# Performance work log

Hardware: AMD Instinct MI355X
Metric: run time of the kernel (lower is better)

The kernel has to match this reference:

```python
import jax, jax.numpy as jnp
import numpy as np

N, D = 16384, 512
MARGIN = 2.0
EPS = 1e-6  # torch TripletMarginLoss default eps added inside pairwise distance


def setup_inputs() -> dict:
    key = jax.random.key(0)
    k1, k2 = jax.random.split(key)
    inputs = jax.random.normal(k1, (N, D), dtype=jnp.float32)
    positive = jax.random.normal(k2, (N, D), dtype=jnp.float32)
    return {"inputs": inputs, "positive": positive}


def reference(inputs, positive):
    # pairwise squared euclidean distances: ||xi||^2 + ||xj||^2 - 2 xi.xj
    sq = jnp.sum(inputs * inputs, axis=1)                      # [n]
    dist2 = sq[:, None] + sq[None, :] - 2.0 * (inputs @ inputs.T)  # [n,n]
    dist = jnp.sqrt(jnp.clip(dist2, 1e-12))                    # [n,n]
    # original does full argsort per row but only uses index 2 (3rd smallest);
    # top_k on negated distances selects the 3 smallest efficiently.
    _, idx3 = jax.lax.top_k(-dist, 3)                          # [n,3]
    negative = inputs[idx3[:, 2]]                              # [n,d]
    # TripletMarginLoss(margin, p=2): mean(relu(||a-p+eps|| - ||a-n+eps|| + m))
    d_ap = jnp.linalg.norm(inputs - positive + EPS, axis=1)
    d_an = jnp.linalg.norm(inputs - negative + EPS, axis=1)
    loss = jnp.mean(jnp.maximum(d_ap - d_an + MARGIN, 0.0))
    return loss
```

## Files before the change

### kernel.cpp

```cpp
#include <hip/hip_runtime.h>
#include <hip/hip_bf16.h>
#include <hip/hip_fp8.h>
#include <stdint.h>

#define NN 16384
#define DD 512
#define MARGINV 2.0f
#define EPSV 1e-6f

#define BJ 32
#define JGROUPS 8
#define JRANGE (NN / JGROUPS)
#define NTILES (JRANGE / BJ)
#define ROWQ 512
#define TILEB (BJ * ROWQ)
#define SQOFF (2 * TILEB)

#define KEYMASK  0xFFFFC000
#define KEYINITF __builtin_bit_cast(float, 0x7F000000)
#define BIASV 640.0f

typedef __attribute__((ext_vector_type(4))) float f32x4;
typedef __attribute__((ext_vector_type(4))) int   i32x4;
typedef __attribute__((ext_vector_type(8))) int   i32x8;

#define UNIT_SCALE 0x7F

__device__ inline void kins3f(float u, float& m0, float& m1, float& m2) {
  m2 = __builtin_amdgcn_fmed3f(m1, m2, u);
  m1 = __builtin_amdgcn_fmed3f(m0, m1, u);
  m0 = fminf(m0, u);
}

extern "C" __global__ __launch_bounds__(256)
void prep_kernel(const float* __restrict__ x, unsigned char* __restrict__ xq,
                 float* __restrict__ sqb, float* __restrict__ out) {
  if (blockIdx.x == 0 && threadIdx.x == 0) out[0] = 0.0f;
  int row  = blockIdx.x * 4 + (threadIdx.x >> 6);
  int lane = threadIdx.x & 63;
  const float* xr = x + (size_t)row * DD + lane * 8;
  f32x4 a = *(const f32x4*)xr;
  f32x4 b = *(const f32x4*)(xr + 4);
  float s = a[0]*a[0]+a[1]*a[1]+a[2]*a[2]+a[3]*a[3]
          + b[0]*b[0]+b[1]*b[1]+b[2]*b[2]+b[3]*b[3];
  #pragma unroll
  for (int off = 1; off < 64; off <<= 1) s += __shfl_xor(s, off, 64);
  unsigned long long pk = 0;
  #pragma unroll
  for (int t = 0; t < 4; ++t) {
    __hip_fp8_e4m3 qa(a[t]), qb(b[t]);
    pk |= ((unsigned long long)qa.__x) << (8 * t);
    pk |= ((unsigned long long)qb.__x) << (8 * (t + 4));
  }
  *(unsigned long long*)(xq + (size_t)row * ROWQ + lane * 8) = pk;
  if (lane == 0) sqb[row] = s + BIASV;
}

extern "C" __global__ __launch_bounds__(256, 2)
void knn_kernel(const unsigned char* __restrict__ xq, const float* __restrict__ sqb,
                int* __restrict__ pk) {
  __shared__ __align__(16) char lds[2 * TILEB + 8192];
  const int tid  = threadIdx.x;
  const int wave = tid >> 6;
  const int lane = tid & 63;
  const int quad = lane >> 4;
  const int r16  = lane & 15;
  const int bi   = blockIdx.x >> 3;
  const int bj   = blockIdx.x & 7;
  const int ibase = bi * 256 + wave * 64;
  const int jbase = bj * JRANGE;

  #pragma unroll
  for (int p = 0; p < 2; ++p) {
    const float* gs = sqb + jbase + p * 1024 + wave * 256 + lane * 4;
    char* ld = lds + SQOFF + p * 4096 + wave * 1024;
    __builtin_amdgcn_global_load_lds((const __attribute__((address_space(1))) void*)gs,
                                     (__attribute__((address_space(3))) void*)ld,
                                     16, 0, 0);
  }

  i32x8 afr[4][4];
  #pragma unroll
  for (int s = 0; s < 4; ++s) {
    const unsigned char* ar = xq + (size_t)(ibase + s * 16 + r16) * ROWQ + quad * 32;
    #pragma unroll
    for (int c = 0; c < 4; ++c)
      afr[s][c] = *(const i32x8*)(ar + c * 128);
  }

  float m0[16], m1[16], m2[16];
  #pragma unroll
  for (int q = 0; q < 16; ++q) { m0[q] = m1[q] = m2[q] = KEYINITF; }

  auto stage = [&](int jt, int buf) {
    const int jrow0 = jbase + jt * BJ;
    #pragma unroll
    for (int p = 0; p < 4; ++p) {
      const int rr = wave * 8 + p * 2;
      const int lr = rr + (lane >> 5);
      const int u  = (lane & 31) ^ (lr & 7);
      const unsigned char* gsrc = xq + (size_t)(jrow0 + lr) * ROWQ + u * 16;
      char* ldst = lds + buf * TILEB + rr * ROWQ;
      __builtin_amdgcn_global_load_lds((const __attribute__((address_space(1))) void*)gsrc,
                                       (__attribute__((address_space(3))) void*)ldst,
                                       16, 0, 0);
    }
  };

  const int sw = r16 & 7;
  stage(0, 0);
  for (int jt = 0; jt < NTILES; ++jt) {
    __syncthreads();
    if (jt + 1 < NTILES) stage(jt + 1, (jt + 1) & 1);
    #pragma unroll
    for (int jh = 0; jh < 2; ++jh) {
      const char* brow = lds + (jt & 1) * TILEB + (jh * 16 + r16) * ROWQ;
      const float sqj = *(const float*)(lds + SQOFF + ((jt * BJ + jh * 16 + r16) << 2));
      f32x4 acc[4] = {{0.f,0.f,0.f,0.f},{0.f,0.f,0.f,0.f},
                      {0.f,0.f,0.f,0.f},{0.f,0.f,0.f,0.f}};
      #pragma unroll
      for (int c = 0; c < 4; ++c) {
        const int g0 = c * 8 + quad * 2;
        i32x4 lo = *(const i32x4*)(brow + ((g0       ^ sw) * 16));
        i32x4 hi = *(const i32x4*)(brow + (((g0 + 1) ^ sw) * 16));
        i32x8 bf = i32x8{lo[0],lo[1],lo[2],lo[3],hi[0],hi[1],hi[2],hi[3]};
        #pragma unroll
        for (int s = 0; s < 4; ++s)
          acc[s] = __builtin_amdgcn_mfma_scale_f32_16x16x128_f8f6f4(
                     afr[s][c], bf, acc[s], 0, 0, 0, UNIT_SCALE, 0, UNIT_SCALE);
      }
      const int j = jbase + jt * BJ + jh * 16 + r16;
      #pragma unroll
      for (int s = 0; s < 4; ++s) {
        #pragma unroll
        for (int r = 0; r < 4; ++r) {
          float v = fmaf(-2.0f, acc[s][r], sqj);
          int   b = (__builtin_bit_cast(int, v) & KEYMASK) | j;
          kins3f(__builtin_bit_cast(float, b), m0[s*4+r], m1[s*4+r], m2[s*4+r]);
        }
      }
    }
  }

  #pragma unroll
  for (int m = 1; m <= 8; m <<= 1) {
    #pragma unroll
    for (int q = 0; q < 16; ++q) {
      float o0 = __shfl_xor(m0[q], m, 64);
      float o1 = __shfl_xor(m1[q], m, 64);
      float o2 = __shfl_xor(m2[q], m, 64);
      kins3f(o0, m0[q], m1[q], m2[q]);
      kins3f(o1, m0[q], m1[q], m2[q]);
      kins3f(o2, m0[q], m1[q], m2[q]);
    }
  }

  #pragma unroll
  for (int q = 0; q < 16; ++q) {
    if (r16 == q) {
      int s  = q >> 2, r = q & 3;
      int gi = ibase + s * 16 + quad * 4 + r;
      int ob = (gi * JGROUPS + bj) * 3;
      pk[ob + 0] = __builtin_bit_cast(int, m0[q]);
      pk[ob + 1] = __builtin_bit_cast(int, m1[q]);
      pk[ob + 2] = __builtin_bit_cast(int, m2[q]);
    }
  }
}

extern "C" __global__ __launch_bounds__(256)
void finalize_kernel(const float* __restrict__ x, const float* __restrict__ pos,
                     const int* __restrict__ pk, float* __restrict__ out) {
  __shared__ float wsum[4];
  int wave = threadIdx.x >> 6;
  int lane = threadIdx.x & 63;
  float acc = 0.f;
  #pragma unroll
  for (int rep = 0; rep < 8; ++rep) {
    int i = rep * 2048 + blockIdx.x * 4 + wave;
    int neg = 0;
    if (lane == 0) {
      float m0 = KEYINITF, m1 = KEYINITF, m2 = KEYINITF;
      #pragma unroll
      for (int s = 0; s < JGROUPS * 3; ++s) {
        kins3f(__builtin_bit_cast(float, pk[i * (JGROUPS * 3) + s]), m0, m1, m2);
      }
      neg = __builtin_bit_cast(int, m2) & 0x3FFF;
    }
    neg = __shfl(neg, 0, 64);
    const float* xr = x   + (size_t)i * DD + lane * 8;
    const float* pr = pos + (size_t)i * DD + lane * 8;
    const float* nr = x   + (size_t)neg * DD + lane * 8;
    f32x4 xa = *(const f32x4*)xr, xb4 = *(const f32x4*)(xr + 4);
    f32x4 pa = *(const f32x4*)pr, pb  = *(const f32x4*)(pr + 4);
    f32x4 na = *(const f32x4*)nr, nb  = *(const f32x4*)(nr + 4);
    float sap = 0.f, san = 0.f;
    #pragma unroll
    for (int k = 0; k < 4; ++k) {
      float d0 = xa[k]  - pa[k] + EPSV; sap = fmaf(d0, d0, sap);
      float d1 = xa[k]  - na[k] + EPSV; san = fmaf(d1, d1, san);
      float d2 = xb4[k] - pb[k] + EPSV; sap = fmaf(d2, d2, sap);
      float d3 = xb4[k] - nb[k] + EPSV; san = fmaf(d3, d3, san);
    }
    #pragma unroll
    for (int off = 1; off < 64; off <<= 1) {
      sap += __shfl_xor(sap, off, 64);
      san += __shfl_xor(san, off, 64);
    }
    if (lane == 0) {
      float l = sqrtf(sap) - sqrtf(san) + MARGINV;
      acc += (l > 0.f ? l : 0.f);
    }
  }
  if (lane == 0) wsum[wave] = acc;
  __syncthreads();
  if (threadIdx.x == 0) {
    atomicAdd(out, (wsum[0] + wsum[1] + wsum[2] + wsum[3]) * (1.0f / NN));
  }
}

extern "C" void kernel_launch(void* const* d_in, const int* in_sizes, int n_in,
                              void* d_out, int out_size, void* d_ws, size_t ws_size,
                              hipStream_t stream) {
  const float* x   = (const float*)d_in[0];
  const float* pos = (const float*)d_in[1];
  char* ws = (char*)d_ws;
  unsigned char* xq  = (unsigned char*)ws;
  float* sqb = (float*)(ws + (size_t)NN * ROWQ);
  int*   pk  = (int*)  (ws + (size_t)NN * ROWQ + (size_t)NN * 4);

  prep_kernel<<<NN / 4, 256, 0, stream>>>(x, xq, sqb, (float*)d_out);
  knn_kernel<<<(NN / 256) * JGROUPS, 256, 0, stream>>>(xq, sqb, pk);
  finalize_kernel<<<512, 256, 0, stream>>>(x, pos, pk, (float*)d_out);
}
```

Before: 237.0 us.

## Track top-2 excluding self, use 8-wave blocks, hardware FP8 pack, deterministic reduce

The kNN kernel now runs 512-thread blocks in which each wave handles 32 rows instead of 64. It masks the diagonal so each row keeps only the two smallest non-self keys instead of three, which removes one med3 per candidate and shrinks register state. It also raises MFMA issue priority with setprio. The prep kernel uses the hardware packed FP8 conversion instead of per-element conversion. Finalize merges the 16 partial keys with a wave shuffle and writes per-block partials that a new single-block reduce kernel sums, replacing the atomic. Self-exclusion assumes the self-distance is always the minimum, which matches the reference's index-2 choice unless there are duplicates or near ties.

```diff
diff --git a/kernel.cpp b/kernel.cpp
--- a/kernel.cpp
+++ b/kernel.cpp
@@ -26,16 +26,14 @@
 
 #define UNIT_SCALE 0x7F
 
-__device__ inline void kins3f(float u, float& m0, float& m1, float& m2) {
-  m2 = __builtin_amdgcn_fmed3f(m1, m2, u);
+__device__ inline void kins2f(float u, float& m0, float& m1) {
   m1 = __builtin_amdgcn_fmed3f(m0, m1, u);
   m0 = fminf(m0, u);
 }
 
 extern "C" __global__ __launch_bounds__(256)
 void prep_kernel(const float* __restrict__ x, unsigned char* __restrict__ xq,
-                 float* __restrict__ sqb, float* __restrict__ out) {
-  if (blockIdx.x == 0 && threadIdx.x == 0) out[0] = 0.0f;
+                 float* __restrict__ sqb) {
   int row  = blockIdx.x * 4 + (threadIdx.x >> 6);
   int lane = threadIdx.x & 63;
   const float* xr = x + (size_t)row * DD + lane * 8;
@@ -45,18 +43,16 @@
           + b[0]*b[0]+b[1]*b[1]+b[2]*b[2]+b[3]*b[3];
   #pragma unroll
   for (int off = 1; off < 64; off <<= 1) s += __shfl_xor(s, off, 64);
-  unsigned long long pk = 0;
-  #pragma unroll
-  for (int t = 0; t < 4; ++t) {
-    __hip_fp8_e4m3 qa(a[t]), qb(b[t]);
-    pk |= ((unsigned long long)qa.__x) << (8 * t);
-    pk |= ((unsigned long long)qb.__x) << (8 * (t + 4));
-  }
-  *(unsigned long long*)(xq + (size_t)row * ROWQ + lane * 8) = pk;
+  unsigned int w0 = (unsigned int)__builtin_amdgcn_cvt_pk_fp8_f32(a[0], a[1], 0, false);
+  w0 = (unsigned int)__builtin_amdgcn_cvt_pk_fp8_f32(a[2], a[3], (int)w0, true);
+  unsigned int w1 = (unsigned int)__builtin_amdgcn_cvt_pk_fp8_f32(b[0], b[1], 0, false);
+  w1 = (unsigned int)__builtin_amdgcn_cvt_pk_fp8_f32(b[2], b[3], (int)w1, true);
+  unsigned long long pk8 = ((unsigned long long)w1 << 32) | (unsigned long long)w0;
+  *(unsigned long long*)(xq + (size_t)row * ROWQ + lane * 8) = pk8;
   if (lane == 0) sqb[row] = s + BIASV;
 }
 
-extern "C" __global__ __launch_bounds__(256, 2)
+extern "C" __global__ __launch_bounds__(512, 4)
 void knn_kernel(const unsigned char* __restrict__ xq, const float* __restrict__ sqb,
                 int* __restrict__ pk) {
   __shared__ __align__(16) char lds[2 * TILEB + 8192];
@@ -67,36 +63,35 @@
   const int r16  = lane & 15;
   const int bi   = blockIdx.x >> 3;
   const int bj   = blockIdx.x & 7;
-  const int ibase = bi * 256 + wave * 64;
+  const int ibase = bi * 256 + wave * 32;
   const int jbase = bj * JRANGE;
 
-  #pragma unroll
-  for (int p = 0; p < 2; ++p) {
-    const float* gs = sqb + jbase + p * 1024 + wave * 256 + lane * 4;
-    char* ld = lds + SQOFF + p * 4096 + wave * 1024;
+  {
+    const float* gs = sqb + jbase + wave * 256 + lane * 4;
+    char* ld = lds + SQOFF + wave * 1024;
     __builtin_amdgcn_global_load_lds((const __attribute__((address_space(1))) void*)gs,
                                      (__attribute__((address_space(3))) void*)ld,
                                      16, 0, 0);
   }
 
-  i32x8 afr[4][4];
-  #pragma unroll
-  for (int s = 0; s < 4; ++s) {
+  i32x8 afr[2][4];
+  #pragma unroll
+  for (int s = 0; s < 2; ++s) {
     const unsigned char* ar = xq + (size_t)(ibase + s * 16 + r16) * ROWQ + quad * 32;
     #pragma unroll
     for (int c = 0; c < 4; ++c)
       afr[s][c] = *(const i32x8*)(ar + c * 128);
   }
 
-  float m0[16], m1[16], m2[16];
-  #pragma unroll
-  for (int q = 0; q < 16; ++q) { m0[q] = m1[q] = m2[q] = KEYINITF; }
+  float m0[8], m1[8];
+  #pragma unroll
+  for (int q = 0; q < 8; ++q) { m0[q] = m1[q] = KEYINITF; }
 
   auto stage = [&](int jt, int buf) {
     const int jrow0 = jbase + jt * BJ;
     #pragma unroll
-    for (int p = 0; p < 4; ++p) {
-      const int rr = wave * 8 + p * 2;
+    for (int p = 0; p < 2; ++p) {
+      const int rr = wave * 4 + p * 2;
       const int lr = rr + (lane >> 5);
       const int u  = (lane & 31) ^ (lr & 7);
       const unsigned char* gsrc = xq + (size_t)(jrow0 + lr) * ROWQ + u * 16;
@@ -112,31 +107,45 @@
   for (int jt = 0; jt < NTILES; ++jt) {
     __syncthreads();
     if (jt + 1 < NTILES) stage(jt + 1, (jt + 1) & 1);
+    const bool diagt = ((bi >> 3) == bj) && ((jt >> 3) == (bi & 7));
     #pragma unroll
     for (int jh = 0; jh < 2; ++jh) {
       const char* brow = lds + (jt & 1) * TILEB + (jh * 16 + r16) * ROWQ;
       const float sqj = *(const float*)(lds + SQOFF + ((jt * BJ + jh * 16 + r16) << 2));
-      f32x4 acc[4] = {{0.f,0.f,0.f,0.f},{0.f,0.f,0.f,0.f},
-                      {0.f,0.f,0.f,0.f},{0.f,0.f,0.f,0.f}};
+      f32x4 acc[2] = {{0.f,0.f,0.f,0.f},{0.f,0.f,0.f,0.f}};
       #pragma unroll
       for (int c = 0; c < 4; ++c) {
         const int g0 = c * 8 + quad * 2;
         i32x4 lo = *(const i32x4*)(brow + ((g0       ^ sw) * 16));
         i32x4 hi = *(const i32x4*)(brow + (((g0 + 1) ^ sw) * 16));
         i32x8 bf = i32x8{lo[0],lo[1],lo[2],lo[3],hi[0],hi[1],hi[2],hi[3]};
-        #pragma unroll
-        for (int s = 0; s < 4; ++s)
+        __builtin_amdgcn_s_setprio(1);
+        #pragma unroll
+        for (int s = 0; s < 2; ++s)
           acc[s] = __builtin_amdgcn_mfma_scale_f32_16x16x128_f8f6f4(
                      afr[s][c], bf, acc[s], 0, 0, 0, UNIT_SCALE, 0, UNIT_SCALE);
+        __builtin_amdgcn_s_setprio(0);
       }
       const int j = jbase + jt * BJ + jh * 16 + r16;
-      #pragma unroll
-      for (int s = 0; s < 4; ++s) {
+      if (diagt) {
+        #pragma unroll
+        for (int s = 0; s < 2; ++s)
         #pragma unroll
         for (int r = 0; r < 4; ++r) {
           float v = fmaf(-2.0f, acc[s][r], sqj);
           int   b = (__builtin_bit_cast(int, v) & KEYMASK) | j;
-          kins3f(__builtin_bit_cast(float, b), m0[s*4+r], m1[s*4+r], m2[s*4+r]);
+          float u = __builtin_bit_cast(float, b);
+          u = (j == (ibase + s * 16 + quad * 4 + r)) ? KEYINITF : u;
+          kins2f(u, m0[s*4+r], m1[s*4+r]);
+        }
+      } else {
+        #pragma unroll
+        for (int s = 0; s < 2; ++s)
+        #pragma unroll
+        for (int r = 0; r < 4; ++r) {
+          float v = fmaf(-2.0f, acc[s][r], sqj);
+          int   b = (__builtin_bit_cast(int, v) & KEYMASK) | j;
+          kins2f(__builtin_bit_cast(float, b), m0[s*4+r], m1[s*4+r]);
         }
       }
     }
@@ -145,49 +154,47 @@
   #pragma unroll
   for (int m = 1; m <= 8; m <<= 1) {
     #pragma unroll
-    for (int q = 0; q < 16; ++q) {
+    for (int q = 0; q < 8; ++q) {
       float o0 = __shfl_xor(m0[q], m, 64);
       float o1 = __shfl_xor(m1[q], m, 64);
-      float o2 = __shfl_xor(m2[q], m, 64);
-      kins3f(o0, m0[q], m1[q], m2[q]);
-      kins3f(o1, m0[q], m1[q], m2[q]);
-      kins3f(o2, m0[q], m1[q], m2[q]);
-    }
-  }
-
-  #pragma unroll
-  for (int q = 0; q < 16; ++q) {
+      kins2f(o0, m0[q], m1[q]);
+      kins2f(o1, m0[q], m1[q]);
+    }
+  }
+
+  #pragma unroll
+  for (int q = 0; q < 8; ++q) {
     if (r16 == q) {
       int s  = q >> 2, r = q & 3;
       int gi = ibase + s * 16 + quad * 4 + r;
-      int ob = (gi * JGROUPS + bj) * 3;
+      int ob = (gi * JGROUPS + bj) * 2;
       pk[ob + 0] = __builtin_bit_cast(int, m0[q]);
       pk[ob + 1] = __builtin_bit_cast(int, m1[q]);
-      pk[ob + 2] = __builtin_bit_cast(int, m2[q]);
     }
   }
 }
 
 extern "C" __global__ __launch_bounds__(256)
 void finalize_kernel(const float* __restrict__ x, const float* __restrict__ pos,
-                     const int* __restrict__ pk, float* __restrict__ out) {
+                     const int* __restrict__ pk, float* __restrict__ partial) {
   __shared__ float wsum[4];
   int wave = threadIdx.x >> 6;
   int lane = threadIdx.x & 63;
   float acc = 0.f;
   #pragma unroll
-  for (int rep = 0; rep < 8; ++rep) {
-    int i = rep * 2048 + blockIdx.x * 4 + wave;
-    int neg = 0;
-    if (lane == 0) {
-      float m0 = KEYINITF, m1 = KEYINITF, m2 = KEYINITF;
-      #pragma unroll
-      for (int s = 0; s < JGROUPS * 3; ++s) {
-        kins3f(__builtin_bit_cast(float, pk[i * (JGROUPS * 3) + s]), m0, m1, m2);
-      }
-      neg = __builtin_bit_cast(int, m2) & 0x3FFF;
-    }
-    neg = __shfl(neg, 0, 64);
+  for (int rep = 0; rep < 2; ++rep) {
+    int i = rep * 8192 + blockIdx.x * 4 + wave;
+    float m0 = (lane < 16) ? __builtin_bit_cast(float, pk[i * 16 + lane]) : KEYINITF;
+    float m1 = KEYINITF;
+    #pragma unroll
+    for (int m = 1; m <= 8; m <<= 1) {
+      float o0 = __shfl_xor(m0, m, 64);
+      float o1 = __shfl_xor(m1, m, 64);
+      float t0 = fminf(m0, o0);
+      m1 = fminf(fmaxf(m0, o0), fminf(m1, o1));
+      m0 = t0;
+    }
+    int neg = __shfl(__builtin_bit_cast(int, m1), 0, 64) & 0x3FFF;
     const float* xr = x   + (size_t)i * DD + lane * 8;
     const float* pr = pos + (size_t)i * DD + lane * 8;
     const float* nr = x   + (size_t)neg * DD + lane * 8;
@@ -214,9 +221,21 @@
   }
   if (lane == 0) wsum[wave] = acc;
   __syncthreads();
-  if (threadIdx.x == 0) {
-    atomicAdd(out, (wsum[0] + wsum[1] + wsum[2] + wsum[3]) * (1.0f / NN));
-  }
+  if (threadIdx.x == 0) partial[blockIdx.x] = wsum[0] + wsum[1] + wsum[2] + wsum[3];
+}
+
+extern "C" __global__ __launch_bounds__(256)
+void reduce_kernel(const float* __restrict__ partial, float* __restrict__ out) {
+  __shared__ float wsum[4];
+  int tid = threadIdx.x;
+  float s = 0.f;
+  #pragma unroll
+  for (int k = 0; k < 8; ++k) s += partial[tid + k * 256];
+  #pragma unroll
+  for (int off = 1; off < 64; off <<= 1) s += __shfl_xor(s, off, 64);
+  if ((tid & 63) == 0) wsum[tid >> 6] = s;
+  __syncthreads();
+  if (tid == 0) out[0] = (wsum[0] + wsum[1] + wsum[2] + wsum[3]) * (1.0f / NN);
 }
 
 extern "C" void kernel_launch(void* const* d_in, const int* in_sizes, int n_in,
@@ -225,11 +244,14 @@
   const float* x   = (const float*)d_in[0];
   const float* pos = (const float*)d_in[1];
   char* ws = (char*)d_ws;
-  unsigned char* xq  = (unsigned char*)ws;
-  float* sqb = (float*)(ws + (size_t)NN * ROWQ);
-  int*   pk  = (int*)  (ws + (size_t)NN * ROWQ + (size_t)NN * 4);
-
-  prep_kernel<<<NN / 4, 256, 0, stream>>>(x, xq, sqb, (float*)d_out);
-  knn_kernel<<<(NN / 256) * JGROUPS, 256, 0, stream>>>(xq, sqb, pk);
-  finalize_kernel<<<512, 256, 0, stream>>>(x, pos, pk, (float*)d_out);
-}
+  unsigned char* xq   = (unsigned char*)ws;
+  float* sqb  = (float*)(ws + (size_t)NN * ROWQ);
+  int*   pk   = (int*)  (ws + (size_t)NN * ROWQ + (size_t)NN * 4);
+  float* part = (float*)(ws + (size_t)NN * ROWQ + (size_t)NN * 4
+                            + (size_t)NN * JGROUPS * 2 * 4);
+
+  prep_kernel<<<NN / 4, 256, 0, stream>>>(x, xq, sqb);
+  knn_kernel<<<(NN / 256) * JGROUPS, 512, 0, stream>>>(xq, sqb, pk);
+  finalize_kernel<<<2048, 256, 0, stream>>>(x, pos, pk, part);
+  reduce_kernel<<<1, 256, 0, stream>>>(part, (float*)d_out);
+}
```

Measured after the change: 591.4 us. 150% more time.
